# Optimization experiments

Hardware: AMD Instinct MI355X
Metric: run time of the kernel (lower is better)

The kernel has to match this reference:

```python
import jax, jax.numpy as jnp
import numpy as np

THEA = 0.5
DELTA = 1.5
IGNORE = 255
K = 19  # num classes (len(weights))
LOSS_WEIGHT = 1.0
MIN_PIXELS = 20.0  # class kept only if pixel count > 20
WEIGHTS = jnp.ones((K,), dtype=jnp.float32)
EPS = 1e-12


def setup_inputs() -> dict:
    key = jax.random.key(0)
    k1, k2 = jax.random.split(key)
    n, c, h, w = 4, 32, 512, 1024
    predict = jax.random.normal(k1, (n, c, h, w), dtype=jnp.float32)
    target = jax.random.randint(k2, (n, h, w), 0, K, dtype=jnp.int32)
    return {"predict": predict, "target": target}


def _loss(predict, target):
    n, c, h, w = predict.shape
    # (n,c,h,w) -> (n*h*w, c), matching predict.permute(0,2,3,1)
    feat = jnp.transpose(predict, (0, 2, 3, 1)).reshape(-1, c)
    seg = target.reshape(-1)
    valid_pix = seg != IGNORE
    seg = jnp.where(valid_pix, seg, K).astype(jnp.int32)  # ignored -> extra segment K
    ones = valid_pix.astype(feat.dtype)

    # per-class counts and means (segment reduce replaces the python class loop)
    counts = jax.ops.segment_sum(ones, seg, num_segments=K + 1)[:K]
    sums = jax.ops.segment_sum(feat * ones[:, None], seg, num_segments=K + 1)[:K]
    centers = sums / jnp.maximum(counts, 1.0)[:, None]  # [K, c]
    valid_cls = counts > MIN_PIXELS
    n_cls = jnp.maximum(jnp.sum(valid_cls.astype(feat.dtype)), 1.0)

    # ---- variance term: relu(||mean - x|| - thea)^2, normalized by #positives ----
    ctr_ext = jnp.concatenate([centers, jnp.zeros((1, c), centers.dtype)], axis=0)
    ctr_pix = ctr_ext[seg]  # gather per-pixel center
    res = jnp.sqrt(jnp.sum((ctr_pix - feat) ** 2, axis=1) + EPS)  # [n*h*w]
    r = jax.nn.relu(res - THEA) * ones
    sq = jax.ops.segment_sum(r * r, seg, num_segments=K + 1)[:K]
    pos = jax.ops.segment_sum((r > 0).astype(feat.dtype), seg, num_segments=K + 1)[:K]
    norml = jnp.maximum(jax.lax.stop_gradient(pos), 1.0)  # numpy count in original: no grad
    loss_var = jnp.sum(jnp.where(valid_cls, WEIGHTS * sq / norml, 0.0)) / n_cls

    # ---- pairwise center distance term ----
    diff = centers[:, None, :] - centers[None, :, :]  # [K, K, c]
    dist = jnp.sqrt(jnp.sum(diff * diff, axis=-1) + EPS)
    pair_mask = valid_cls[:, None] & valid_cls[None, :] & ~jnp.eye(K, dtype=bool)
    d = jax.nn.relu(2.0 * DELTA - dist)
    loss_dis = jnp.sum(jnp.where(pair_mask, d * d, 0.0)) / jnp.maximum(n_cls * (n_cls - 1.0), 1.0)

    # ---- regularization term ----
    loss_reg = jnp.sum(jnp.where(valid_cls, jnp.sqrt(jnp.sum(centers * centers, axis=1) + EPS), 0.0)) / n_cls

    return LOSS_WEIGHT * (loss_var + loss_dis + 0.001 * loss_reg)


def reference(predict, target):
    return _loss(predict, target)
```

## Files before the change

### kernel.cpp

```cpp
#include <hip/hip_runtime.h>


#define K_CLS 19
#define C_CH 32
#define HW_SHIFT 19
#define HW_SIZE (1 << HW_SHIFT)
#define EPSF 1e-12f
#define THEA_F 0.5f
#define TWO_DELTA 3.0f
#define MIN_PIX 20.0f

#define OFF_PSUM 0
#define OFF_PCNT 40960
#define OFF_RED  42240
#define OFF_VRED 42880
#define OFF_VPART 42944
#define WS_FLOATS (OFF_VPART + 1024 * 64)

typedef const unsigned int __attribute__((address_space(1)))* GP;
typedef unsigned int __attribute__((address_space(3)))* LP;

__device__ __forceinline__ void atomAddF(float* p, float v) {
  unsafeAtomicAdd(p, v);
}

__global__ __launch_bounds__(256) void k_accum(
    const float* __restrict__ pred, const int* __restrict__ tgt,
    float* __restrict__ ws)
{
  __shared__ float sA[4][K_CLS][64];
  __shared__ float s_w[4][20];
  const int t = threadIdx.x;
  const int w = t >> 6;
  const int lane = t & 63;
  float* colA = &sA[w][0][lane];
#pragma unroll
  for (int k = 0; k < K_CLS; ++k) colA[k << 6] = 0.f;

  if (blockIdx.x < 2048) {
    const int plane = blockIdx.x >> 4;
    const int slab  = blockIdx.x & 15;
    const int n_idx = plane >> 5;
    const int ch    = plane & 31;
    const float* pbase = pred + (((size_t)plane) << HW_SHIFT) + ((size_t)slab << 15);
    const int*   tbase = tgt  + (((size_t)n_idx) << HW_SHIFT) + ((size_t)slab << 15);

    float4 vA = *reinterpret_cast<const float4*>(pbase + t * 4);
    int4   cA = *reinterpret_cast<const int4*>(tbase + t * 4);
#pragma unroll 1
    for (int it = 0; it < 32; ++it) {
      float4 vB; int4 cB;
      if (it + 1 < 32) {
        vB = *reinterpret_cast<const float4*>(pbase + (it + 1) * 1024 + t * 4);
        cB = *reinterpret_cast<const int4*>(tbase + (it + 1) * 1024 + t * 4);
      }
      const float x[4] = {vA.x, vA.y, vA.z, vA.w};
      const int   s[4] = {cA.x, cA.y, cA.z, cA.w};
      const int   k0 = min((unsigned)s[0], 18u), k1 = min((unsigned)s[1], 18u);
      const int   k2 = min((unsigned)s[2], 18u), k3 = min((unsigned)s[3], 18u);
      const float v0 = ((unsigned)s[0] < K_CLS) ? x[0] : 0.f;
      const float v1 = ((unsigned)s[1] < K_CLS) ? x[1] : 0.f;
      const float v2 = ((unsigned)s[2] < K_CLS) ? x[2] : 0.f;
      const float v3 = ((unsigned)s[3] < K_CLS) ? x[3] : 0.f;
      colA[k0 << 6] += v0;
      colA[k1 << 6] += v1;
      colA[k2 << 6] += v2;
      colA[k3 << 6] += v3;
      vA = vB; cA = cB;
    }

    float acc[K_CLS];
#pragma unroll
    for (int k = 0; k < K_CLS; ++k) acc[k] = colA[k << 6];
#pragma unroll
    for (int k = 0; k < K_CLS; ++k) {
      float s = acc[k];
#pragma unroll
      for (int m = 1; m < 64; m <<= 1) s += __shfl_xor(s, m, 64);
      acc[k] = s;
    }
#pragma unroll
    for (int k = 0; k < K_CLS; ++k)
      if (lane == k) s_w[w][k] = acc[k];
    __syncthreads();
    if (t < K_CLS) {
      const int slot = n_idx * 16 + slab;
      ws[OFF_PSUM + ch * (64 * 20) + slot * 20 + t] =
          s_w[0][t] + s_w[1][t] + s_w[2][t] + s_w[3][t];
    }
  } else {
    const int idx = blockIdx.x - 2048;
    const int n_idx = idx >> 4;
    const int slab  = idx & 15;
    const int* tbase = tgt + (((size_t)n_idx) << HW_SHIFT) + ((size_t)slab << 15);

#pragma unroll 1
    for (int it = 0; it < 32; ++it) {
      const int4 c4 = *reinterpret_cast<const int4*>(tbase + it * 1024 + t * 4);
      const int s[4] = {c4.x, c4.y, c4.z, c4.w};
      const int k0 = min((unsigned)s[0], 18u), k1 = min((unsigned)s[1], 18u);
      const int k2 = min((unsigned)s[2], 18u), k3 = min((unsigned)s[3], 18u);
      colA[k0 << 6] += ((unsigned)s[0] < K_CLS) ? 1.f : 0.f;
      colA[k1 << 6] += ((unsigned)s[1] < K_CLS) ? 1.f : 0.f;
      colA[k2 << 6] += ((unsigned)s[2] < K_CLS) ? 1.f : 0.f;
      colA[k3 << 6] += ((unsigned)s[3] < K_CLS) ? 1.f : 0.f;
    }

    float acc[K_CLS];
#pragma unroll
    for (int k = 0; k < K_CLS; ++k) acc[k] = colA[k << 6];
#pragma unroll
    for (int k = 0; k < K_CLS; ++k) {
      float s = acc[k];
#pragma unroll
      for (int m = 1; m < 64; m <<= 1) s += __shfl_xor(s, m, 64);
      acc[k] = s;
    }
#pragma unroll
    for (int k = 0; k < K_CLS; ++k)
      if (lane == k) s_w[w][k] = acc[k];
    __syncthreads();
    if (t < K_CLS) {
      const int slot = n_idx * 16 + slab;
      ws[OFF_PCNT + slot * 20 + t] = s_w[0][t] + s_w[1][t] + s_w[2][t] + s_w[3][t];
    }
  }
}

__global__ __launch_bounds__(64) void k_reduce(float* __restrict__ ws)
{
  const int o = blockIdx.x;
  const int lane = threadIdx.x;
  float a;
  if (o < C_CH * K_CLS) {
    const int ch = o / K_CLS, k = o - ch * K_CLS;
    a = ws[OFF_PSUM + ch * (64 * 20) + lane * 20 + k];
  } else {
    a = ws[OFF_PCNT + lane * 20 + (o - C_CH * K_CLS)];
  }
#pragma unroll
  for (int m = 1; m < 64; m <<= 1) a += __shfl_xor(a, m, 64);
  if (lane == 0) ws[OFF_RED + o] = a;
}

__global__ __launch_bounds__(256) void k_var(
    const float* __restrict__ pred, const int* __restrict__ tgt,
    float* __restrict__ ws)
{
  __shared__ float s_buf[4][2][16][64];
  __shared__ int   s_cls[4][2][64];
  __shared__ float s_ctr[C_CH][K_CLS];
  __shared__ float s_w[4][40];

  const int t = threadIdx.x;
  const int w = t >> 6;
  const int lane = t & 63;

  for (int i = t; i < C_CH * K_CLS; i += 256) {
    const int k = i % K_CLS;
    (&s_ctr[0][0])[i] = ws[OFF_RED + i] / fmaxf(ws[OFF_RED + C_CH * K_CLS + k], 1.f);
  }
  __syncthreads();

  const size_t P0 = (size_t)blockIdx.x * 2048;
  const int n_idx = (int)(P0 >> HW_SHIFT);
  const int hw0 = (int)(P0 & (HW_SIZE - 1));

#define VSTAGE(s_)                                                            \
  {                                                                           \
    const int p_ = (s_) & 1, pxw_ = (s_) >> 1;                                \
    const int pw_ = hw0 + w * 512 + pxw_ * 64;                                \
    const int cb_ = p_ * 16;                                                  \
    _Pragma("unroll")                                                         \
    for (int q = 0; q < 4; ++q) {                                             \
      const int ch_ = cb_ + q * 4 + (lane >> 4);                              \
      const float* gp = pred + (((size_t)(n_idx * C_CH + ch_)) << HW_SHIFT)   \
                        + pw_ + (lane & 15) * 4;                              \
      __builtin_amdgcn_global_load_lds((GP)gp, (LP)&s_buf[w][p_][q * 4][0],   \
                                       16, 0, 0);                             \
    }                                                                         \
    if (p_ == 0 && lane < 16) {                                               \
      const int* gt = tgt + (((size_t)n_idx) << HW_SHIFT) + pw_ + lane * 4;   \
      __builtin_amdgcn_global_load_lds((GP)gt, (LP)&s_cls[w][pxw_ & 1][0],    \
                                       16, 0, 0);                             \
    }                                                                         \
  }

  float acc_sq[K_CLS], acc_pos[K_CLS];
#pragma unroll
  for (int k = 0; k < K_CLS; ++k) { acc_sq[k] = 0.f; acc_pos[k] = 0.f; }

  int  ci = 0, sc = 0;
  bool vld = false;
  float d2 = 0.f;

  VSTAGE(0)
#pragma unroll 1
  for (int s = 0; s < 16; ++s) {
    if (s < 15) {
      VSTAGE(s + 1)
      if (s & 1) asm volatile("s_waitcnt vmcnt(5)" ::: "memory");
      else       asm volatile("s_waitcnt vmcnt(4)" ::: "memory");
    } else {
      asm volatile("s_waitcnt vmcnt(0)" ::: "memory");
    }
    __builtin_amdgcn_sched_barrier(0);

    const int p = s & 1, pxw = s >> 1, cb = p * 16;
    if (p == 0) {
      ci = s_cls[w][pxw & 1][lane];
      vld = (unsigned)ci < K_CLS;
      sc = vld ? ci : 0;
      d2 = 0.f;
    }
#pragma unroll
    for (int cc = 0; cc < 16; ++cc) {
      const float x = s_buf[w][p][cc][lane];
      const float d = s_ctr[cb + cc][sc] - x;
      d2 = fmaf(d, d, d2);
    }
    if (p == 1) {
      const float r = sqrtf(d2 + EPSF) - THEA_F;
      const bool act = vld && (r > 0.f);
      const float rr = act ? r * r : 0.f;
      const float pp = act ? 1.f : 0.f;
#pragma unroll
      for (int k = 0; k < K_CLS; ++k) {
        const bool b = (sc == k);
        acc_sq[k]  += b ? rr : 0.f;
        acc_pos[k] += b ? pp : 0.f;
      }
    }
  }
#undef VSTAGE

#pragma unroll
  for (int k = 0; k < K_CLS; ++k) {
    float a = acc_sq[k], b = acc_pos[k];
#pragma unroll
    for (int m = 1; m < 64; m <<= 1) {
      a += __shfl_xor(a, m, 64);
      b += __shfl_xor(b, m, 64);
    }
    acc_sq[k] = a; acc_pos[k] = b;
  }
#pragma unroll
  for (int k = 0; k < K_CLS; ++k)
    if (lane == k) { s_w[w][k] = acc_sq[k]; s_w[w][20 + k] = acc_pos[k]; }
  __syncthreads();
  if (t < K_CLS) {
    float* vp = ws + OFF_VPART + (size_t)blockIdx.x * 64;
    vp[t]         = s_w[0][t] + s_w[1][t] + s_w[2][t] + s_w[3][t];
    vp[K_CLS + t] = s_w[0][20 + t] + s_w[1][20 + t] + s_w[2][20 + t] + s_w[3][20 + t];
  }
}

__global__ __launch_bounds__(256) void k_vred(float* __restrict__ ws)
{
  const int o = blockIdx.x;
  const int t = threadIdx.x;
  float a = 0.f;
#pragma unroll
  for (int r = 0; r < 4; ++r)
    a += ws[OFF_VPART + (size_t)(t + r * 256) * 64 + o];
#pragma unroll
  for (int m = 1; m < 64; m <<= 1) a += __shfl_xor(a, m, 64);
  __shared__ float s[4];
  if ((t & 63) == 0) s[t >> 6] = a;
  __syncthreads();
  if (t == 0) ws[OFF_VRED + o] = s[0] + s[1] + s[2] + s[3];
}

__global__ __launch_bounds__(1024) void k_final(
    float* __restrict__ ws, float* __restrict__ out)
{
  __shared__ float s_ctr[C_CH * K_CLS];
  __shared__ float s_valid[K_CLS];
  __shared__ float s_red[3];
  __shared__ float s_ncls;
  const int t = threadIdx.x;
  if (t < 3) s_red[t] = 0.f;
  if (t < K_CLS) s_valid[t] = (ws[OFF_RED + C_CH * K_CLS + t] > MIN_PIX) ? 1.f : 0.f;
  for (int i = t; i < C_CH * K_CLS; i += 1024) {
    const int k = i % K_CLS;
    s_ctr[i] = ws[OFF_RED + i] / fmaxf(ws[OFF_RED + C_CH * K_CLS + k], 1.f);
  }
  __syncthreads();

  if (t == 0) {
    float n = 0.f;
    for (int k = 0; k < K_CLS; ++k) n += s_valid[k];
    s_ncls = fmaxf(n, 1.f);
  }
  if (t < K_CLS && s_valid[t] > 0.f) {
    const float sq  = ws[OFF_VRED + t];
    const float pos = ws[OFF_VRED + K_CLS + t];
    atomAddF(&s_red[0], sq / fmaxf(pos, 1.f));
    float nn = 0.f;
#pragma unroll
    for (int ch = 0; ch < C_CH; ++ch) {
      const float cv = s_ctr[ch * K_CLS + t];
      nn = fmaf(cv, cv, nn);
    }
    atomAddF(&s_red[2], sqrtf(nn + EPSF));
  }
  if (t < K_CLS * K_CLS) {
    const int a = t / K_CLS, b = t - (t / K_CLS) * K_CLS;
    if (a != b && s_valid[a] > 0.f && s_valid[b] > 0.f) {
      float dd = 0.f;
#pragma unroll
      for (int ch = 0; ch < C_CH; ++ch) {
        const float df = s_ctr[ch * K_CLS + a] - s_ctr[ch * K_CLS + b];
        dd = fmaf(df, df, dd);
      }
      const float dist = sqrtf(dd + EPSF);
      const float d = fmaxf(TWO_DELTA - dist, 0.f);
      if (d > 0.f) atomAddF(&s_red[1], d * d);
    }
  }
  __syncthreads();
  if (t == 0) {
    const float n = s_ncls;
    out[0] = s_red[0] / n
           + s_red[1] / fmaxf(n * (n - 1.f), 1.f)
           + 0.001f * s_red[2] / n;
  }
}

extern "C" void kernel_launch(void* const* d_in, const int* in_sizes, int n_in,
                              void* d_out, int out_size, void* d_ws, size_t ws_size,
                              hipStream_t stream) {
  const float* pred = (const float*)d_in[0];
  const int*   tgt  = (const int*)d_in[1];
  float* ws  = (float*)d_ws;
  float* out = (float*)d_out;
  const int P = in_sizes[1];
  const int nBlocksVar = P / 2048;

  k_accum <<<2048 + 64, 256, 0, stream>>>(pred, tgt, ws);
  k_reduce<<<C_CH * K_CLS + K_CLS, 64, 0, stream>>>(ws);
  k_var   <<<nBlocksVar, 256, 0, stream>>>(pred, tgt, ws);
  k_vred  <<<2 * K_CLS, 256, 0, stream>>>(ws);
  k_final <<<1, 1024, 0, stream>>>(ws, out);
}
```

Before: 436.0 us.

## Rewrite variance pass with register centers, bpermute lookup and norm expansion

```diff
diff --git a/kernel.cpp b/kernel.cpp
--- a/kernel.cpp
+++ b/kernel.cpp
@@ -15,13 +15,14 @@
 #define OFF_RED  42240
 #define OFF_VRED 42880
 #define OFF_VPART 42944
-#define WS_FLOATS (OFF_VPART + 1024 * 64)
-
-typedef const unsigned int __attribute__((address_space(1)))* GP;
-typedef unsigned int __attribute__((address_space(3)))* LP;
+#define WS_FLOATS (OFF_VPART + 2048 * 64)
 
 __device__ __forceinline__ void atomAddF(float* p, float v) {
   unsafeAtomicAdd(p, v);
+}
+
+__device__ __forceinline__ float bperm(float v, int byteidx) {
+  return __int_as_float(__builtin_amdgcn_ds_bpermute(byteidx, __float_as_int(v)));
 }
 
 __global__ __launch_bounds__(256) void k_accum(
@@ -147,92 +148,72 @@
     const float* __restrict__ pred, const int* __restrict__ tgt,
     float* __restrict__ ws)
 {
-  __shared__ float s_buf[4][2][16][64];
-  __shared__ int   s_cls[4][2][64];
-  __shared__ float s_ctr[C_CH][K_CLS];
+  __shared__ float s_red[640];
   __shared__ float s_w[4][40];
-
   const int t = threadIdx.x;
   const int w = t >> 6;
   const int lane = t & 63;
 
-  for (int i = t; i < C_CH * K_CLS; i += 256) {
-    const int k = i % K_CLS;
-    (&s_ctr[0][0])[i] = ws[OFF_RED + i] / fmaxf(ws[OFF_RED + C_CH * K_CLS + k], 1.f);
-  }
-  __syncthreads();
-
-  const size_t P0 = (size_t)blockIdx.x * 2048;
-  const int n_idx = (int)(P0 >> HW_SHIFT);
-  const int hw0 = (int)(P0 & (HW_SIZE - 1));
-
-#define VSTAGE(s_)                                                            \
-  {                                                                           \
-    const int p_ = (s_) & 1, pxw_ = (s_) >> 1;                                \
-    const int pw_ = hw0 + w * 512 + pxw_ * 64;                                \
-    const int cb_ = p_ * 16;                                                  \
-    _Pragma("unroll")                                                         \
-    for (int q = 0; q < 4; ++q) {                                             \
-      const int ch_ = cb_ + q * 4 + (lane >> 4);                              \
-      const float* gp = pred + (((size_t)(n_idx * C_CH + ch_)) << HW_SHIFT)   \
-                        + pw_ + (lane & 15) * 4;                              \
-      __builtin_amdgcn_global_load_lds((GP)gp, (LP)&s_buf[w][p_][q * 4][0],   \
-                                       16, 0, 0);                             \
-    }                                                                         \
-    if (p_ == 0 && lane < 16) {                                               \
-      const int* gt = tgt + (((size_t)n_idx) << HW_SHIFT) + pw_ + lane * 4;   \
-      __builtin_amdgcn_global_load_lds((GP)gt, (LP)&s_cls[w][pxw_ & 1][0],    \
-                                       16, 0, 0);                             \
-    }                                                                         \
+  for (int i = t; i < 627; i += 256) s_red[i] = ws[OFF_RED + i];
+  __syncthreads();
+
+  const float invc = (lane < K_CLS) ? 1.f / fmaxf(s_red[608 + lane], 1.f) : 0.f;
+  float ctrreg[C_CH];
+  float c2reg = 0.f;
+#pragma unroll
+  for (int c = 0; c < C_CH; ++c) {
+    ctrreg[c] = (lane < K_CLS) ? s_red[c * K_CLS + lane] * invc : 0.f;
+    c2reg = fmaf(ctrreg[c], ctrreg[c], c2reg);
+  }
+
+  const size_t px0 = (size_t)blockIdx.x * 1024;
+  const int n_idx = (int)(px0 >> HW_SHIFT);
+  const int hw = (int)(px0 & (HW_SIZE - 1)) + t * 4;
+  const float* pb = pred + (((size_t)(n_idx * C_CH)) << HW_SHIFT) + hw;
+
+  const int4 c4 = *reinterpret_cast<const int4*>(tgt + ((size_t)n_idx << HW_SHIFT) + hw);
+  const int cls[4] = {c4.x, c4.y, c4.z, c4.w};
+  bool vl[4]; int sc[4]; int idx[4];
+#pragma unroll
+  for (int j = 0; j < 4; ++j) {
+    vl[j] = (unsigned)cls[j] < K_CLS;
+    sc[j] = vl[j] ? cls[j] : 0;
+    idx[j] = sc[j] << 2;
+  }
+
+  float dot[4] = {0.f, 0.f, 0.f, 0.f};
+  float nrm[4] = {0.f, 0.f, 0.f, 0.f};
+#pragma unroll
+  for (int c = 0; c < C_CH; ++c) {
+    const float4 x = *reinterpret_cast<const float4*>(pb + ((size_t)c << HW_SHIFT));
+    const float cv0 = bperm(ctrreg[c], idx[0]);
+    const float cv1 = bperm(ctrreg[c], idx[1]);
+    const float cv2 = bperm(ctrreg[c], idx[2]);
+    const float cv3 = bperm(ctrreg[c], idx[3]);
+    dot[0] = fmaf(x.x, cv0, dot[0]);  nrm[0] = fmaf(x.x, x.x, nrm[0]);
+    dot[1] = fmaf(x.y, cv1, dot[1]);  nrm[1] = fmaf(x.y, x.y, nrm[1]);
+    dot[2] = fmaf(x.z, cv2, dot[2]);  nrm[2] = fmaf(x.z, x.z, nrm[2]);
+    dot[3] = fmaf(x.w, cv3, dot[3]);  nrm[3] = fmaf(x.w, x.w, nrm[3]);
   }
 
   float acc_sq[K_CLS], acc_pos[K_CLS];
 #pragma unroll
   for (int k = 0; k < K_CLS; ++k) { acc_sq[k] = 0.f; acc_pos[k] = 0.f; }
-
-  int  ci = 0, sc = 0;
-  bool vld = false;
-  float d2 = 0.f;
-
-  VSTAGE(0)
-#pragma unroll 1
-  for (int s = 0; s < 16; ++s) {
-    if (s < 15) {
-      VSTAGE(s + 1)
-      if (s & 1) asm volatile("s_waitcnt vmcnt(5)" ::: "memory");
-      else       asm volatile("s_waitcnt vmcnt(4)" ::: "memory");
-    } else {
-      asm volatile("s_waitcnt vmcnt(0)" ::: "memory");
-    }
-    __builtin_amdgcn_sched_barrier(0);
-
-    const int p = s & 1, pxw = s >> 1, cb = p * 16;
-    if (p == 0) {
-      ci = s_cls[w][pxw & 1][lane];
-      vld = (unsigned)ci < K_CLS;
-      sc = vld ? ci : 0;
-      d2 = 0.f;
-    }
-#pragma unroll
-    for (int cc = 0; cc < 16; ++cc) {
-      const float x = s_buf[w][p][cc][lane];
-      const float d = s_ctr[cb + cc][sc] - x;
-      d2 = fmaf(d, d, d2);
-    }
-    if (p == 1) {
-      const float r = sqrtf(d2 + EPSF) - THEA_F;
-      const bool act = vld && (r > 0.f);
-      const float rr = act ? r * r : 0.f;
-      const float pp = act ? 1.f : 0.f;
-#pragma unroll
-      for (int k = 0; k < K_CLS; ++k) {
-        const bool b = (sc == k);
-        acc_sq[k]  += b ? rr : 0.f;
-        acc_pos[k] += b ? pp : 0.f;
-      }
-    }
-  }
-#undef VSTAGE
+#pragma unroll
+  for (int j = 0; j < 4; ++j) {
+    const float c2j = bperm(c2reg, idx[j]);
+    const float d2 = fmaxf(nrm[j] - 2.f * dot[j] + c2j, 0.f);
+    const float r = sqrtf(d2 + EPSF) - THEA_F;
+    const bool act = vl[j] && (r > 0.f);
+    const float rr = act ? r * r : 0.f;
+    const float pp = act ? 1.f : 0.f;
+#pragma unroll
+    for (int k = 0; k < K_CLS; ++k) {
+      const bool b = (sc[j] == k);
+      acc_sq[k]  += b ? rr : 0.f;
+      acc_pos[k] += b ? pp : 0.f;
+    }
+  }
 
 #pragma unroll
   for (int k = 0; k < K_CLS; ++k) {
@@ -261,7 +242,7 @@
   const int t = threadIdx.x;
   float a = 0.f;
 #pragma unroll
-  for (int r = 0; r < 4; ++r)
+  for (int r = 0; r < 8; ++r)
     a += ws[OFF_VPART + (size_t)(t + r * 256) * 64 + o];
 #pragma unroll
   for (int m = 1; m < 64; m <<= 1) a += __shfl_xor(a, m, 64);
@@ -335,7 +316,7 @@
   float* ws  = (float*)d_ws;
   float* out = (float*)d_out;
   const int P = in_sizes[1];
-  const int nBlocksVar = P / 2048;
+  const int nBlocksVar = P / 1024;
 
   k_accum <<<2048 + 64, 256, 0, stream>>>(pred, tgt, ws);
   k_reduce<<<C_CH * K_CLS + K_CLS, 64, 0, stream>>>(ws);
```

New measurement: 441.7 us. About the same (+1.3%).
